# Kernel tuning notes

Hardware: AMD Instinct MI355X
Metric: run time of the kernel (lower is better)

## Reference

```python
import jax, jax.numpy as jnp
import numpy as np

SCALE_WEIGHT = 0.5 ** 0.5
B, C, T, S = 8, 512, 2048, 2048


def setup_inputs() -> dict:
    key = jax.random.key(0)
    ks = jax.random.split(key, 6)
    return {
        "base_target_emb": jax.random.normal(ks[0], (B, C, T, 1), dtype=jnp.float32),
        "input_from_dec": jax.random.normal(ks[1], (B, C, T, 1), dtype=jnp.float32),
        "encoder_out_top": jax.random.normal(ks[2], (B, C, S), dtype=jnp.float32),
        "encoder_out_combine": jax.random.normal(ks[3], (B, C, S), dtype=jnp.float32),
        "W": jax.random.normal(ks[4], (C, C), dtype=jnp.float32) * (1.0 / np.sqrt(C)),
        "b": jax.random.normal(ks[5], (C,), dtype=jnp.float32) * 0.01,
    }


def reference(base_target_emb, input_from_dec, encoder_out_top, encoder_out_combine, W, b):
    # seq_linear: per-token Linear over the channel dim. torch Linear: h = x @ W.T + b, W is [out,in]
    x = input_from_dec[..., 0]                                # [B,C,T]
    preatt = jnp.einsum('oc,bct->bot', W, x) + b[None, :, None]  # [B,C,T]
    target = (base_target_emb[..., 0] + preatt) * SCALE_WEIGHT   # [B,C,T]
    pre_attn = jnp.einsum('bct,bcs->bts', target, encoder_out_top)  # [B,T,S]
    attn = jax.nn.softmax(pre_attn, axis=2)                      # [B,T,S]
    ctx = jnp.einsum('bts,bcs->btc', attn, encoder_out_combine)  # [B,T,C]
    context_output = jnp.transpose(ctx, (0, 2, 1))[..., None]    # [B,C,T,1]
    return context_output, attn
```

## Files before the change

kernel.cpp:

```cpp
#include <hip/hip_runtime.h>
#include <cstddef>
#include <cstdint>

#define SCALE_WEIGHT 0.70710678118654752440f

static constexpr int B_ = 8, C_ = 512, T_ = 2048, S_ = 2048;
static constexpr size_t BCT_ = (size_t)B_ * C_ * T_;
static constexpr size_t BTS_ = (size_t)B_ * T_ * S_;

typedef _Float16 half_t;
typedef half_t half8  __attribute__((ext_vector_type(8)));
typedef half_t half4v __attribute__((ext_vector_type(4)));
typedef float  floatx4 __attribute__((ext_vector_type(4)));

__device__ __forceinline__ void gload_lds16(const void* g, void* l) {
    __builtin_amdgcn_global_load_lds(
        (const __attribute__((address_space(1))) void*)g,
        (__attribute__((address_space(3))) void*)l, 16, 0, 0);
}

__global__ __launch_bounds__(256) void pre_kernel(
    const float* __restrict__ x, const float* __restrict__ top,
    const float* __restrict__ comb, const float* __restrict__ W,
    half_t* __restrict__ xT, half_t* __restrict__ topT,
    half_t* __restrict__ combh, half_t* __restrict__ Wh)
{
    const int z = blockIdx.z;
    if (z < 16) {
        __shared__ float tile[64][65];
        const float* in = (z < 8) ? x : top;
        half_t* outp = (z < 8) ? xT : topT;
        const int b  = z & 7;
        const int r0 = blockIdx.y * 64, c0 = blockIdx.x * 64;
        const float* ib = in + (size_t)b * C_ * T_;
        half_t* ob = outp + (size_t)b * C_ * T_;
        const int t  = threadIdx.x;
        const int rr = t >> 4, cq = t & 15;
        #pragma unroll
        for (int i = 0; i < 4; ++i) {
            const int r = rr + i * 16;
            float4 v = *(const float4*)&ib[(size_t)(r0 + r) * T_ + c0 + cq * 4];
            tile[cq * 4 + 0][r] = v.x;
            tile[cq * 4 + 1][r] = v.y;
            tile[cq * 4 + 2][r] = v.z;
            tile[cq * 4 + 3][r] = v.w;
        }
        __syncthreads();
        const int cw = t >> 4, rq = (t & 15) * 4;
        #pragma unroll
        for (int i = 0; i < 4; ++i) {
            const int c = cw + i * 16;
            half4v h = {(half_t)tile[c][rq + 0], (half_t)tile[c][rq + 1],
                        (half_t)tile[c][rq + 2], (half_t)tile[c][rq + 3]};
            *(half4v*)&ob[(size_t)(c0 + c) * C_ + r0 + rq] = h;
        }
    } else {
        const int n4a = (int)((size_t)B_ * C_ * S_ / 4);
        const int n4tot = n4a + C_ * C_ / 4;
        const int planeT = 32 * 8 * 256;
        for (int i = (blockIdx.y * 32 + blockIdx.x) * 256 + threadIdx.x;
             i < n4tot; i += planeT) {
            const float4* src; half4v* dst; int j;
            if (i < n4a) { src = (const float4*)comb; dst = (half4v*)combh; j = i; }
            else         { src = (const float4*)W;    dst = (half4v*)Wh;    j = i - n4a; }
            float4 v = src[j];
            dst[j] = (half4v){(half_t)v.x, (half_t)v.y, (half_t)v.z, (half_t)v.w};
        }
    }
}

template<int EPI>
__global__ __launch_bounds__(256) void gemm_f16_db_kernel(
    const half_t* __restrict__ A, const half_t* __restrict__ Bm,
    float* __restrict__ Cout, half_t* __restrict__ CoutH,
    const float* __restrict__ base, const float* __restrict__ bias,
    int M, int N, int K, size_t sA, size_t sB, size_t sC)
{
    __shared__ __align__(128) half_t As[2][128 * 64];
    __shared__ __align__(128) half_t Bs[2][128 * 64];

    const int tid  = threadIdx.x;
    const int lane = tid & 63, w = tid >> 6;
    const int wr = w >> 1, wc = w & 1;
    const int b  = blockIdx.z;
    const int m0 = blockIdx.y * 128, n0 = blockIdx.x * 128;

    const half_t* Ab = A  + (size_t)b * sA;
    const half_t* Bb = Bm + (size_t)b * sB;

    const int lr = lane >> 3;
    const int sw = (lane & 7) ^ lr;
    const half_t* aG[4]; const half_t* bG[4];
    int dOff[4];
    #pragma unroll
    for (int i = 0; i < 4; ++i) {
        const int r = w * 32 + i * 8 + lr;
        aG[i] = Ab + (size_t)(m0 + r) * K + sw * 8;
        bG[i] = Bb + (size_t)(n0 + r) * K + sw * 8;
        dOff[i] = (w * 32 + i * 8) * 128;
    }

    const int fr = lane & 15, kg = lane >> 4;
    int aoff[4], boff[4];
    #pragma unroll
    for (int mi = 0; mi < 4; ++mi) {
        const int m = wr * 64 + mi * 16 + fr;
        aoff[mi] = m * 128 + ((kg ^ (m & 7)) << 4);
    }
    #pragma unroll
    for (int nj = 0; nj < 4; ++nj) {
        const int n = wc * 64 + nj * 16 + fr;
        boff[nj] = n * 128 + ((kg ^ (n & 7)) << 4);
    }

    floatx4 acc[4][4];
    #pragma unroll
    for (int mi = 0; mi < 4; ++mi)
        #pragma unroll
        for (int nj = 0; nj < 4; ++nj)
            acc[mi][nj] = (floatx4){0.f, 0.f, 0.f, 0.f};

    auto STAGE = [&](int t, int pg) {
        const int k0 = t * 64;
        char* Ad = (char*)As[pg];
        char* Bd = (char*)Bs[pg];
        #pragma unroll
        for (int i = 0; i < 4; ++i) {
            gload_lds16(aG[i] + k0, Ad + dOff[i]);
            gload_lds16(bG[i] + k0, Bd + dOff[i]);
        }
    };

    auto COMPUTE = [&](int pg) {
        const char* Ar = (const char*)As[pg];
        const char* Br = (const char*)Bs[pg];
        #pragma unroll
        for (int kk = 0; kk < 2; ++kk) {
            half8 af[4], bf[4];
            #pragma unroll
            for (int mi = 0; mi < 4; ++mi)
                af[mi] = *(const half8*)(Ar + (aoff[mi] ^ (kk << 6)));
            #pragma unroll
            for (int nj = 0; nj < 4; ++nj)
                bf[nj] = *(const half8*)(Br + (boff[nj] ^ (kk << 6)));
            #pragma unroll
            for (int mi = 0; mi < 4; ++mi)
                #pragma unroll
                for (int nj = 0; nj < 4; ++nj)
                    acc[mi][nj] = __builtin_amdgcn_mfma_f32_16x16x32_f16(
                        af[mi], bf[nj], acc[mi][nj], 0, 0, 0);
        }
    };

    const int NT = K >> 6;
    STAGE(0, 0);
    int cur = 0;
    for (int t = 0; t < NT - 1; ++t) {
        STAGE(t + 1, cur ^ 1);
        asm volatile("s_waitcnt vmcnt(8)" ::: "memory");
        __builtin_amdgcn_s_barrier();
        __builtin_amdgcn_sched_barrier(0);
        COMPUTE(cur);
        asm volatile("s_waitcnt lgkmcnt(0)" ::: "memory");
        __builtin_amdgcn_sched_barrier(0);
        __builtin_amdgcn_s_barrier();
        __builtin_amdgcn_sched_barrier(0);
        cur ^= 1;
    }
    asm volatile("s_waitcnt vmcnt(0)" ::: "memory");
    __builtin_amdgcn_s_barrier();
    __builtin_amdgcn_sched_barrier(0);
    COMPUTE(cur);

    if constexpr (EPI == 0) {
        float* Cb = Cout + (size_t)b * sC;
        #pragma unroll
        for (int mi = 0; mi < 4; ++mi) {
            const int row = m0 + wr * 64 + mi * 16 + (lane >> 4) * 4;
            #pragma unroll
            for (int nj = 0; nj < 4; ++nj) {
                const int col = n0 + wc * 64 + nj * 16 + (lane & 15);
                #pragma unroll
                for (int r = 0; r < 4; ++r)
                    Cb[(size_t)(row + r) * N + col] = acc[mi][nj][r];
            }
        }
    } else {
        half_t* Cb = CoutH + (size_t)b * sC;
        #pragma unroll
        for (int nj = 0; nj < 4; ++nj) {
            const int col = n0 + wc * 64 + nj * 16 + (lane & 15);
            const float bn = bias[col];
            const float* bp = base + ((size_t)b * N + col) * (size_t)M;
            #pragma unroll
            for (int mi = 0; mi < 4; ++mi) {
                const int row = m0 + wr * 64 + mi * 16 + (lane >> 4) * 4;
                #pragma unroll
                for (int r = 0; r < 4; ++r) {
                    float v = (acc[mi][nj][r] + bn + bp[row + r]) * SCALE_WEIGHT;
                    Cb[(size_t)(row + r) * N + col] = (half_t)v;
                }
            }
        }
    }
}

__global__ __launch_bounds__(256) void k3_softmax_kernel(
    float* __restrict__ logits, half_t* __restrict__ attnh)
{
    float* p = logits + (size_t)blockIdx.x * S_;
    half4v* ph = (half4v*)(attnh + (size_t)blockIdx.x * S_);
    const int tid = threadIdx.x;
    float4 v0 = *(const float4*)&p[tid * 4];
    float4 v1 = *(const float4*)&p[tid * 4 + 1024];

    float mx = fmaxf(fmaxf(fmaxf(v0.x, v0.y), fmaxf(v0.z, v0.w)),
                     fmaxf(fmaxf(v1.x, v1.y), fmaxf(v1.z, v1.w)));
    #pragma unroll
    for (int off = 32; off; off >>= 1)
        mx = fmaxf(mx, __shfl_xor(mx, off));

    __shared__ float sm[4];
    __shared__ float ss[4];
    const int wid = tid >> 6, lane = tid & 63;
    if (lane == 0) sm[wid] = mx;
    __syncthreads();
    const float rmax = fmaxf(fmaxf(sm[0], sm[1]), fmaxf(sm[2], sm[3]));

    float e[8];
    e[0] = __expf(v0.x - rmax); e[1] = __expf(v0.y - rmax);
    e[2] = __expf(v0.z - rmax); e[3] = __expf(v0.w - rmax);
    e[4] = __expf(v1.x - rmax); e[5] = __expf(v1.y - rmax);
    e[6] = __expf(v1.z - rmax); e[7] = __expf(v1.w - rmax);

    float sum = 0.f;
    #pragma unroll
    for (int i = 0; i < 8; ++i) sum += e[i];
    #pragma unroll
    for (int off = 32; off; off >>= 1)
        sum += __shfl_xor(sum, off);
    if (lane == 0) ss[wid] = sum;
    __syncthreads();
    const float inv = 1.f / (ss[0] + ss[1] + ss[2] + ss[3]);

    float4 r0, r1;
    r0.x = e[0] * inv; r0.y = e[1] * inv; r0.z = e[2] * inv; r0.w = e[3] * inv;
    r1.x = e[4] * inv; r1.y = e[5] * inv; r1.z = e[6] * inv; r1.w = e[7] * inv;
    *(float4*)&p[tid * 4] = r0;
    *(float4*)&p[tid * 4 + 1024] = r1;
    ph[tid]       = (half4v){(half_t)r0.x, (half_t)r0.y, (half_t)r0.z, (half_t)r0.w};
    ph[tid + 256] = (half4v){(half_t)r1.x, (half_t)r1.y, (half_t)r1.z, (half_t)r1.w};
}

extern "C" void kernel_launch(void* const* d_in, const int* in_sizes, int n_in,
                              void* d_out, int out_size, void* d_ws, size_t ws_size,
                              hipStream_t stream) {
    const float* base = (const float*)d_in[0];
    const float* x    = (const float*)d_in[1];
    const float* top  = (const float*)d_in[2];
    const float* comb = (const float*)d_in[3];
    const float* W    = (const float*)d_in[4];
    const float* bias = (const float*)d_in[5];

    float* out    = (float*)d_out;
    float* ctx    = out;
    float* logits = out + BCT_;

    half_t* xT   = (half_t*)d_out;
    half_t* topT = xT + BCT_;

    half_t* attnh = (half_t*)d_ws;
    half_t* tgtT  = attnh;
    half_t* combh = attnh + BTS_;
    half_t* Wh    = combh + (size_t)B_ * C_ * S_;

    pre_kernel<<<dim3(32, 8, 17), 256, 0, stream>>>(
        x, top, comb, W, xT, topT, combh, Wh);

    gemm_f16_db_kernel<1><<<dim3(C_ / 128, T_ / 128, B_), 256, 0, stream>>>(
        xT, Wh, nullptr, tgtT, base, bias,
        T_, C_, C_, (size_t)T_ * C_, 0, (size_t)T_ * C_);

    gemm_f16_db_kernel<0><<<dim3(S_ / 128, T_ / 128, B_), 256, 0, stream>>>(
        tgtT, topT, logits, nullptr, nullptr, nullptr,
        T_, S_, C_, (size_t)T_ * C_, (size_t)S_ * C_, (size_t)T_ * S_);

    k3_softmax_kernel<<<dim3(B_ * T_), 256, 0, stream>>>(logits, attnh);

    gemm_f16_db_kernel<0><<<dim3(T_ / 128, C_ / 128, B_), 256, 0, stream>>>(
        combh, attnh, ctx, nullptr, nullptr, nullptr,
        C_, T_, S_, (size_t)C_ * S_, (size_t)T_ * S_, (size_t)C_ * T_);
}
```

Measured before the change: 215.7 us.

## Switch GEMM to 4-stage LDS pipeline with 32-wide K tiles

Restructures the shared GEMM kernel from a double-buffered 64-wide K tile to a four-slot ring of 32-wide K tiles, keeping three stages of global-to-LDS loads in flight. The LDS swizzle and per-thread load addressing change to match the narrower 64-byte rows. The aim is to hide global memory latency better. In exchange there are more barriers per unit of K, and each iteration has less MFMA work to cover them.

```diff
diff --git a/kernel.cpp b/kernel.cpp
--- a/kernel.cpp
+++ b/kernel.cpp
@@ -70,14 +70,13 @@
 }
 
 template<int EPI>
-__global__ __launch_bounds__(256) void gemm_f16_db_kernel(
+__global__ __launch_bounds__(256) void gemm_d3_kernel(
     const half_t* __restrict__ A, const half_t* __restrict__ Bm,
     float* __restrict__ Cout, half_t* __restrict__ CoutH,
     const float* __restrict__ base, const float* __restrict__ bias,
     int M, int N, int K, size_t sA, size_t sB, size_t sC)
 {
-    __shared__ __align__(128) half_t As[2][128 * 64];
-    __shared__ __align__(128) half_t Bs[2][128 * 64];
+    __shared__ __align__(128) char smem[65536];
 
     const int tid  = threadIdx.x;
     const int lane = tid & 63, w = tid >> 6;
@@ -88,29 +87,25 @@
     const half_t* Ab = A  + (size_t)b * sA;
     const half_t* Bb = Bm + (size_t)b * sB;
 
-    const int lr = lane >> 3;
-    const int sw = (lane & 7) ^ lr;
-    const half_t* aG[4]; const half_t* bG[4];
-    int dOff[4];
-    #pragma unroll
-    for (int i = 0; i < 4; ++i) {
-        const int r = w * 32 + i * 8 + lr;
-        aG[i] = Ab + (size_t)(m0 + r) * K + sw * 8;
-        bG[i] = Bb + (size_t)(n0 + r) * K + sw * 8;
-        dOff[i] = (w * 32 + i * 8) * 128;
-    }
-
-    const int fr = lane & 15, kg = lane >> 4;
+    const int lr  = lane >> 2;
+    const int ks8 = ((lane & 3) ^ (lr & 3)) << 3;
+    const half_t* aG0 = Ab + (size_t)(m0 + w * 32 +      lr) * K + ks8;
+    const half_t* aG1 = Ab + (size_t)(m0 + w * 32 + 16 + lr) * K + ks8;
+    const half_t* bG0 = Bb + (size_t)(n0 + w * 32 +      lr) * K + ks8;
+    const half_t* bG1 = Bb + (size_t)(n0 + w * 32 + 16 + lr) * K + ks8;
+    const int dO0 = (w * 32) * 64, dO1 = (w * 32 + 16) * 64;
+
+    const int fr = lane & 15, kg = lane >> 4, q4 = kg * 4;
     int aoff[4], boff[4];
     #pragma unroll
     for (int mi = 0; mi < 4; ++mi) {
         const int m = wr * 64 + mi * 16 + fr;
-        aoff[mi] = m * 128 + ((kg ^ (m & 7)) << 4);
+        aoff[mi] = m * 64 + ((kg ^ (m & 3)) << 4);
     }
     #pragma unroll
     for (int nj = 0; nj < 4; ++nj) {
         const int n = wc * 64 + nj * 16 + fr;
-        boff[nj] = n * 128 + ((kg ^ (n & 7)) << 4);
+        boff[nj] = 32768 + n * 64 + ((kg ^ (n & 3)) << 4);
     }
 
     floatx4 acc[4][4];
@@ -120,66 +115,65 @@
         for (int nj = 0; nj < 4; ++nj)
             acc[mi][nj] = (floatx4){0.f, 0.f, 0.f, 0.f};
 
-    auto STAGE = [&](int t, int pg) {
-        const int k0 = t * 64;
-        char* Ad = (char*)As[pg];
-        char* Bd = (char*)Bs[pg];
-        #pragma unroll
-        for (int i = 0; i < 4; ++i) {
-            gload_lds16(aG[i] + k0, Ad + dOff[i]);
-            gload_lds16(bG[i] + k0, Bd + dOff[i]);
-        }
+    auto STAGE = [&](int t) {
+        const int k0 = t * 32;
+        char* s = smem + (t & 3) * 8192;
+        gload_lds16(aG0 + k0, s + dO0);
+        gload_lds16(aG1 + k0, s + dO1);
+        gload_lds16(bG0 + k0, s + 32768 + dO0);
+        gload_lds16(bG1 + k0, s + 32768 + dO1);
     };
 
-    auto COMPUTE = [&](int pg) {
-        const char* Ar = (const char*)As[pg];
-        const char* Br = (const char*)Bs[pg];
-        #pragma unroll
-        for (int kk = 0; kk < 2; ++kk) {
-            half8 af[4], bf[4];
-            #pragma unroll
-            for (int mi = 0; mi < 4; ++mi)
-                af[mi] = *(const half8*)(Ar + (aoff[mi] ^ (kk << 6)));
+    auto COMPUTE = [&](int t) {
+        const char* s = smem + (t & 3) * 8192;
+        half8 af[4], bf[4];
+        #pragma unroll
+        for (int mi = 0; mi < 4; ++mi) af[mi] = *(const half8*)(s + aoff[mi]);
+        #pragma unroll
+        for (int nj = 0; nj < 4; ++nj) bf[nj] = *(const half8*)(s + boff[nj]);
+        #pragma unroll
+        for (int mi = 0; mi < 4; ++mi)
             #pragma unroll
             for (int nj = 0; nj < 4; ++nj)
-                bf[nj] = *(const half8*)(Br + (boff[nj] ^ (kk << 6)));
-            #pragma unroll
-            for (int mi = 0; mi < 4; ++mi)
-                #pragma unroll
-                for (int nj = 0; nj < 4; ++nj)
-                    acc[mi][nj] = __builtin_amdgcn_mfma_f32_16x16x32_f16(
-                        af[mi], bf[nj], acc[mi][nj], 0, 0, 0);
-        }
+                acc[mi][nj] = __builtin_amdgcn_mfma_f32_16x16x32_f16(
+                    af[mi], bf[nj], acc[mi][nj], 0, 0, 0);
     };
 
-    const int NT = K >> 6;
-    STAGE(0, 0);
-    int cur = 0;
-    for (int t = 0; t < NT - 1; ++t) {
-        STAGE(t + 1, cur ^ 1);
-        asm volatile("s_waitcnt vmcnt(8)" ::: "memory");
+    const int NT = K >> 5;
+    STAGE(0); STAGE(1); STAGE(2);
+    #pragma unroll 1
+    for (int t = 0; t < NT - 3; ++t) {
+        STAGE(t + 3);
+        asm volatile("s_waitcnt vmcnt(12)" ::: "memory");
         __builtin_amdgcn_s_barrier();
         __builtin_amdgcn_sched_barrier(0);
-        COMPUTE(cur);
+        COMPUTE(t);
         asm volatile("s_waitcnt lgkmcnt(0)" ::: "memory");
         __builtin_amdgcn_sched_barrier(0);
         __builtin_amdgcn_s_barrier();
         __builtin_amdgcn_sched_barrier(0);
-        cur ^= 1;
-    }
+    }
+    asm volatile("s_waitcnt vmcnt(8)" ::: "memory");
+    __builtin_amdgcn_s_barrier();
+    __builtin_amdgcn_sched_barrier(0);
+    COMPUTE(NT - 3);
+    asm volatile("s_waitcnt vmcnt(4)" ::: "memory");
+    __builtin_amdgcn_s_barrier();
+    __builtin_amdgcn_sched_barrier(0);
+    COMPUTE(NT - 2);
     asm volatile("s_waitcnt vmcnt(0)" ::: "memory");
     __builtin_amdgcn_s_barrier();
     __builtin_amdgcn_sched_barrier(0);
-    COMPUTE(cur);
+    COMPUTE(NT - 1);
 
     if constexpr (EPI == 0) {
         float* Cb = Cout + (size_t)b * sC;
         #pragma unroll
         for (int mi = 0; mi < 4; ++mi) {
-            const int row = m0 + wr * 64 + mi * 16 + (lane >> 4) * 4;
+            const int row = m0 + wr * 64 + mi * 16 + q4;
             #pragma unroll
             for (int nj = 0; nj < 4; ++nj) {
-                const int col = n0 + wc * 64 + nj * 16 + (lane & 15);
+                const int col = n0 + wc * 64 + nj * 16 + fr;
                 #pragma unroll
                 for (int r = 0; r < 4; ++r)
                     Cb[(size_t)(row + r) * N + col] = acc[mi][nj][r];
@@ -189,12 +183,12 @@
         half_t* Cb = CoutH + (size_t)b * sC;
         #pragma unroll
         for (int nj = 0; nj < 4; ++nj) {
-            const int col = n0 + wc * 64 + nj * 16 + (lane & 15);
+            const int col = n0 + wc * 64 + nj * 16 + fr;
             const float bn = bias[col];
             const float* bp = base + ((size_t)b * N + col) * (size_t)M;
             #pragma unroll
             for (int mi = 0; mi < 4; ++mi) {
-                const int row = m0 + wr * 64 + mi * 16 + (lane >> 4) * 4;
+                const int row = m0 + wr * 64 + mi * 16 + q4;
                 #pragma unroll
                 for (int r = 0; r < 4; ++r) {
                     float v = (acc[mi][nj][r] + bn + bp[row + r]) * SCALE_WEIGHT;
@@ -277,17 +271,17 @@
     pre_kernel<<<dim3(32, 8, 17), 256, 0, stream>>>(
         x, top, comb, W, xT, topT, combh, Wh);
 
-    gemm_f16_db_kernel<1><<<dim3(C_ / 128, T_ / 128, B_), 256, 0, stream>>>(
+    gemm_d3_kernel<1><<<dim3(C_ / 128, T_ / 128, B_), 256, 0, stream>>>(
         xT, Wh, nullptr, tgtT, base, bias,
         T_, C_, C_, (size_t)T_ * C_, 0, (size_t)T_ * C_);
 
-    gemm_f16_db_kernel<0><<<dim3(S_ / 128, T_ / 128, B_), 256, 0, stream>>>(
+    gemm_d3_kernel<0><<<dim3(S_ / 128, T_ / 128, B_), 256, 0, stream>>>(
         tgtT, topT, logits, nullptr, nullptr, nullptr,
         T_, S_, C_, (size_t)T_ * C_, (size_t)S_ * C_, (size_t)T_ * S_);
 
     k3_softmax_kernel<<<dim3(B_ * T_), 256, 0, stream>>>(logits, attnh);
 
-    gemm_f16_db_kernel<0><<<dim3(T_ / 128, C_ / 128, B_), 256, 0, stream>>>(
+    gemm_d3_kernel<0><<<dim3(T_ / 128, C_ / 128, B_), 256, 0, stream>>>(
         combh, attnh, ctx, nullptr, nullptr, nullptr,
         C_, T_, S_, (size_t)C_ * S_, (size_t)T_ * S_, (size_t)C_ * T_);
 }
```

Measured after the change: 217.8 us. About the same (+1.0%).
